# Kernel optimization log

Hardware: AMD Instinct MI355X
Metric: run time of the kernel (lower is better)

## Reference

```python
import jax, jax.numpy as jnp
import numpy as np

N, T, D, H = 2, 2048, 1024, 16
DH = D // H  # per-head dim = 64


def setup_inputs() -> dict:
    key = jax.random.key(0)
    k1, k2, k3, k4 = jax.random.split(key, 4)
    x = jax.random.normal(k1, (N, T, D), dtype=jnp.float32)
    W = jax.random.normal(k2, (D, 3 * D), dtype=jnp.float32) * (D ** -0.5)
    proj_w = jax.random.normal(k3, (D, D), dtype=jnp.float32) * (D ** -0.5)
    proj_b = jax.random.normal(k4, (D,), dtype=jnp.float32) * 0.02
    return {"x": x, "W": W, "proj_w": proj_w, "proj_b": proj_b}


def reference(x, W, proj_w, proj_b):
    n, t, d = x.shape
    qkv = x @ W                                   # [N,T,3D]
    q, k, v = jnp.split(qkv, 3, axis=-1)          # each [N,T,D]
    def heads(a):
        return a.reshape(n, t, H, DH).transpose(0, 2, 1, 3)  # [N,H,T,DH]
    q, k, v = heads(q), heads(k), heads(v)
    scale = DH ** -0.5
    scores = jnp.einsum('nhtd,nhsd->nhts', q, k) * scale      # [N,H,T,T]
    causal = jnp.tril(jnp.ones((t, t), dtype=bool))
    scores = jnp.where(causal, scores, jnp.finfo(scores.dtype).min)
    w = jax.nn.softmax(scores, axis=-1)
    out = jnp.einsum('nhts,nhsd->nhtd', w, v)                 # [N,H,T,DH]
    out = out.transpose(0, 2, 1, 3).reshape(n, t, d)          # [N,T,D]
    return out @ proj_w.T + proj_b
```

## Files before the change

kernel.cpp:

```cpp
#include <hip/hip_runtime.h>
#include <hip/hip_bf16.h>
#include <stdint.h>

#define N_B 2
#define T_S 2048
#define D_M 1024
#define H_N 16
#define D_H 64

typedef __bf16 bf16_t;
typedef __bf16 bf16x8 __attribute__((ext_vector_type(8)));
typedef float f32x4 __attribute__((ext_vector_type(4)));

__device__ __forceinline__ void async_ld16(const void* g, void* lds_uniform_base) {
  __builtin_amdgcn_global_load_lds(
      (const __attribute__((address_space(1))) uint32_t*)(uintptr_t)g,
      (__attribute__((address_space(3))) uint32_t*)(uintptr_t)lds_uniform_base,
      16, 0, 0);
}

__global__ __launch_bounds__(256) void cvt_kernel(const float* __restrict__ in,
                                                  bf16_t* __restrict__ out, int n4) {
  int i = blockIdx.x * blockDim.x + threadIdx.x;
  if (i < n4) {
    float4 v = ((const float4*)in)[i];
    union { bf16_t b[4]; uint64_t u; } o;
    o.b[0] = (bf16_t)v.x; o.b[1] = (bf16_t)v.y;
    o.b[2] = (bf16_t)v.z; o.b[3] = (bf16_t)v.w;
    *(uint64_t*)(out + (size_t)i * 4) = o.u;
  }
}

__global__ __launch_bounds__(256) void transpose_cvt_kernel(const float* __restrict__ in,
                                                            bf16_t* __restrict__ out,
                                                            int R, int C) {
  __shared__ float tile[32][33];
  int bx = blockIdx.x * 32;
  int by = blockIdx.y * 32;
  int tx = threadIdx.x, ty = threadIdx.y;
#pragma unroll
  for (int i = 0; i < 32; i += 8)
    tile[ty + i][tx] = in[(size_t)(by + ty + i) * C + bx + tx];
  __syncthreads();
#pragma unroll
  for (int i = 0; i < 32; i += 8)
    out[(size_t)(bx + ty + i) * R + by + tx] = (bf16_t)tile[tx][ty + i];
}

template <int MODE>
__global__ __launch_bounds__(256) void gemm_bt_kernel(
    const bf16_t* __restrict__ A, const bf16_t* __restrict__ Bt,
    bf16_t* __restrict__ Qo, bf16_t* __restrict__ Ko, bf16_t* __restrict__ Vto,
    const float* __restrict__ bias, float* __restrict__ Co,
    int nbx, int cpx) {
  __shared__ bf16_t As[128 * 32];
  __shared__ bf16_t Bs[128 * 32];
  const int tid = threadIdx.x;
  const int lane = tid & 63;
  const int wid = tid >> 6;
  const int wr = wid >> 1, wc = wid & 1;
  const int g = lane >> 4, lr = lane & 15;
  const int d_ = blockIdx.x;
  const int orig = (d_ & 7) * cpx + (d_ >> 3);
  const int brow = (orig / nbx) * 128;
  const int bcol = (orig % nbx) * 128;

  f32x4 acc[4][4] = {};

  for (int k0 = 0; k0 < 1024; k0 += 32) {
#pragma unroll
    for (int q = 0; q < 2; ++q) {
      int idx = wid * 128 + q * 64 + lane;
      int row = idx >> 2, part = (idx & 3) * 8;
      async_ld16(A + (size_t)(brow + row) * 1024 + k0 + part,
                 &As[(wid * 128 + q * 64) * 8]);
      async_ld16(Bt + (size_t)(bcol + row) * 1024 + k0 + part,
                 &Bs[(wid * 128 + q * 64) * 8]);
    }
    __syncthreads();
    bf16x8 af[4], bfr[4];
#pragma unroll
    for (int i = 0; i < 4; ++i) {
      af[i]  = *(const bf16x8*)&As[(wr * 64 + i * 16 + lr) * 32 + g * 8];
      bfr[i] = *(const bf16x8*)&Bs[(wc * 64 + i * 16 + lr) * 32 + g * 8];
    }
#pragma unroll
    for (int i = 0; i < 4; ++i)
#pragma unroll
      for (int j = 0; j < 4; ++j)
        acc[i][j] = __builtin_amdgcn_mfma_f32_16x16x32_bf16(af[i], bfr[j], acc[i][j], 0, 0, 0);
    __syncthreads();
  }

#pragma unroll
  for (int i = 0; i < 4; ++i) {
    int row0 = brow + wr * 64 + i * 16 + g * 4;
#pragma unroll
    for (int j = 0; j < 4; ++j) {
      int col = bcol + wc * 64 + j * 16 + lr;
#pragma unroll
      for (int r = 0; r < 4; ++r) {
        int row = row0 + r;
        float v = acc[i][j][r];
        if (MODE == 0) {
          int n = row >> 11, t = row & (T_S - 1);
          int which = col >> 10, d = col & (D_M - 1);
          int h = d >> 6, dh = d & 63;
          if (which == 0)
            Qo[((size_t)(n * H_N + h) * T_S + t) * D_H + dh] = (bf16_t)v;
          else if (which == 1)
            Ko[((size_t)(n * H_N + h) * T_S + t) * D_H + dh] = (bf16_t)v;
          else
            Vto[((size_t)(n * H_N + h) * D_H + dh) * T_S + t] = (bf16_t)v;
        } else {
          Co[(size_t)row * D_M + col] = v + bias[col];
        }
      }
    }
  }
}

__global__ __launch_bounds__(256) void attn_kernel(const bf16_t* __restrict__ Q,
                                                   const bf16_t* __restrict__ K,
                                                   const bf16_t* __restrict__ Vt,
                                                   bf16_t* __restrict__ O) {
  __shared__ bf16_t Ks[2][4096];
  __shared__ bf16_t Vs[2][4096];
  __shared__ bf16_t Ps[4][1024];

  const int tid = threadIdx.x;
  const int lane = tid & 63;
  const int w = tid >> 6;
  const int g = lane >> 4, lr = lane & 15;

  const int d_ = blockIdx.x;
  const int x = d_ & 7;
  const int s = d_ >> 3;
  const int hs = s & 3, j_ = s >> 2;
  const int t_ = j_ >> 3, m_ = j_ & 7;
  const int qc = (t_ == 0) ? (31 - m_) : (t_ == 1) ? (16 + m_)
               : (t_ == 2) ? (15 - m_) : m_;
  const int nh = x * 4 + hs;
  const bf16_t* Qg = Q + (size_t)nh * T_S * D_H;
  const char* Kb = (const char*)(K + (size_t)nh * T_S * D_H);
  const char* Vb = (const char*)(Vt + (size_t)nh * D_H * T_S);
  const int n = nh >> 4, h = nh & 15;

  const int c0 = (w * 2 + 0) * 64 + lane;
  const int c1 = (w * 2 + 1) * 64 + lane;
  const int r0 = c0 >> 3, cb0 = (c0 & 7) * 16, sw0 = (r0 & 7) << 4;
  const int r1 = c1 >> 3, cb1 = (c1 & 7) * 16, sw1 = (r1 & 7) << 4;
  const int koff0 = r0 * 128 + (cb0 ^ sw0), koff1 = r1 * 128 + (cb1 ^ sw1);
  const int voff0 = r0 * 4096 + (cb0 ^ sw0), voff1 = r1 * 4096 + (cb1 ^ sw1);
  const int lds0 = (w * 2 + 0) * 1024, lds1 = (w * 2 + 1) * 1024;

  const int q0 = qc * 64 + w * 16;
  const int nt = qc + 1;

  bf16x8 qf[2];
#pragma unroll
  for (int ks = 0; ks < 2; ++ks) {
    bf16x8 t = *(const bf16x8*)(Qg + (size_t)(q0 + lr) * D_H + ks * 32 + g * 8);
#pragma unroll
    for (int e = 0; e < 8; ++e) t[e] = (bf16_t)((float)t[e] * 0.125f);
    qf[ks] = t;
  }

  bf16x8 onesf;
#pragma unroll
  for (int e = 0; e < 8; ++e) onesf[e] = (bf16_t)1.0f;

  f32x4 o_acc[4] = {};
  f32x4 lacc = {};

  auto issue = [&](int t, int b) {
    const char* kt_ = Kb + (size_t)t * 8192;
    const char* vt_ = Vb + (size_t)t * 128;
    async_ld16(kt_ + koff0, (char*)Ks[b] + lds0);
    async_ld16(kt_ + koff1, (char*)Ks[b] + lds1);
    async_ld16(vt_ + voff0, (char*)Vs[b] + lds0);
    async_ld16(vt_ + voff1, (char*)Vs[b] + lds1);
  };

  auto compute = [&](int kt, int b, bool domask) {
    f32x4 s_[4];
    __builtin_amdgcn_s_setprio(1);
#pragma unroll
    for (int j = 0; j < 4; ++j) {
      f32x4 a = {};
#pragma unroll
      for (int ks = 0; ks < 2; ++ks) {
        int row = j * 16 + lr;
        int cb = (ks * 32 + g * 8) * 2;
        bf16x8 kf = *(const bf16x8*)((char*)Ks[b] + ((row * 128 + cb) ^ ((row & 7) << 4)));
        a = __builtin_amdgcn_mfma_f32_16x16x32_bf16(qf[ks], kf, a, 0, 0, 0);
      }
      s_[j] = a;
    }
    __builtin_amdgcn_s_setprio(0);

    if (domask) {
#pragma unroll
      for (int j = 0; j < 4; ++j)
#pragma unroll
        for (int r = 0; r < 4; ++r) {
          int kabs = kt * 64 + j * 16 + lr;
          int qabs = q0 + g * 4 + r;
          if (kabs > qabs) s_[j][r] = -1.0e30f;
        }
    }

#pragma unroll
    for (int j = 0; j < 4; ++j)
#pragma unroll
      for (int r = 0; r < 4; ++r) {
        float sv = fminf(s_[j][r] * 1.442695041f, 50.f);
        float p = __builtin_amdgcn_exp2f(sv);
        int row = g * 4 + r;
        int cb = (j * 16 + lr) * 2;
        *(bf16_t*)((char*)Ps[w] + ((row * 128 + cb) ^ ((row & 7) << 4))) = (bf16_t)p;
      }

    bf16x8 pf[2];
#pragma unroll
    for (int ks = 0; ks < 2; ++ks) {
      int cb = (ks * 32 + g * 8) * 2;
      pf[ks] = *(const bf16x8*)((char*)Ps[w] + ((lr * 128 + cb) ^ ((lr & 7) << 4)));
    }
    __builtin_amdgcn_s_setprio(1);
#pragma unroll
    for (int d = 0; d < 4; ++d) {
#pragma unroll
      for (int ks = 0; ks < 2; ++ks) {
        int row = d * 16 + lr;
        int cb = (ks * 32 + g * 8) * 2;
        bf16x8 vf = *(const bf16x8*)((char*)Vs[b] + ((row * 128 + cb) ^ ((row & 7) << 4)));
        o_acc[d] = __builtin_amdgcn_mfma_f32_16x16x32_bf16(pf[ks], vf, o_acc[d], 0, 0, 0);
      }
    }
#pragma unroll
    for (int ks = 0; ks < 2; ++ks)
      lacc = __builtin_amdgcn_mfma_f32_16x16x32_bf16(pf[ks], onesf, lacc, 0, 0, 0);
    __builtin_amdgcn_s_setprio(0);
  };

  issue(0, 0);
  int buf = 0;
  for (int kt = 0; kt < nt; ++kt) {
    asm volatile("s_waitcnt vmcnt(0)" ::: "memory");
    __builtin_amdgcn_s_barrier();
    __builtin_amdgcn_sched_barrier(0);
    if (kt + 1 < nt) issue(kt + 1, buf ^ 1);
    compute(kt, buf, kt == nt - 1);
    buf ^= 1;
  }

#pragma unroll
  for (int r = 0; r < 4; ++r) {
    int t = q0 + g * 4 + r;
    float inv = 1.f / lacc[r];
#pragma unroll
    for (int d = 0; d < 4; ++d)
      O[(size_t)(n * T_S + t) * D_M + h * D_H + d * 16 + lr] = (bf16_t)(o_acc[d][r] * inv);
  }
}

extern "C" void kernel_launch(void* const* d_in, const int* in_sizes, int n_in,
                              void* d_out, int out_size, void* d_ws, size_t ws_size,
                              hipStream_t stream) {
  const float* x  = (const float*)d_in[0];
  const float* W  = (const float*)d_in[1];
  const float* pw = (const float*)d_in[2];
  const float* pb = (const float*)d_in[3];
  float* out = (float*)d_out;

  char* ws = (char*)d_ws;
  bf16_t* x_bf = (bf16_t*)(ws);
  bf16_t* Wt   = (bf16_t*)(ws + (8ull  << 20));
  bf16_t* pwb  = (bf16_t*)(ws + (14ull << 20));
  bf16_t* Qh   = (bf16_t*)(ws + (16ull << 20));
  bf16_t* Kh   = (bf16_t*)(ws + (24ull << 20));
  bf16_t* Vth  = (bf16_t*)(ws + (32ull << 20));
  bf16_t* Oa   = (bf16_t*)(ws + (40ull << 20));

  cvt_kernel<<<4096, 256, 0, stream>>>(x, x_bf, (4096 * 1024) / 4);
  transpose_cvt_kernel<<<dim3(96, 32), dim3(32, 8), 0, stream>>>(W, Wt, 1024, 3072);
  cvt_kernel<<<1024, 256, 0, stream>>>(pw, pwb, (1024 * 1024) / 4);

  gemm_bt_kernel<0><<<768, 256, 0, stream>>>(x_bf, Wt, Qh, Kh, Vth, nullptr, nullptr, 24, 96);

  attn_kernel<<<1024, 256, 0, stream>>>(Qh, Kh, Vth, Oa);

  gemm_bt_kernel<1><<<256, 256, 0, stream>>>(Oa, pwb, nullptr, nullptr, nullptr, pb, out, 8, 32);
}
```

Measured before the change: 116.1 us.

## Rework attention with 32x32 MFMA, register-resident P and split-K wave pairs

The attention kernel moves from 16x16x32 to 32x32x16 bf16 MFMA tiles. Each pair of waves now shares 32 query rows and splits the 64-key tile in half, with a final LDS reduction to merge the partial outputs and row sums. The softmax probabilities are repacked in registers with cross-half shuffles instead of a round trip through a per-wave LDS buffer. The row sum is accumulated with scalar adds instead of an extra MFMA against a ones vector. This is meant to cut LDS traffic and MFMA issue overhead, at the cost of the epilogue reduction, extra syncs and more register pressure, with an occupancy hint added to launch bounds.

```diff
diff --git a/kernel.cpp b/kernel.cpp
--- a/kernel.cpp
+++ b/kernel.cpp
@@ -11,6 +11,7 @@
 typedef __bf16 bf16_t;
 typedef __bf16 bf16x8 __attribute__((ext_vector_type(8)));
 typedef float f32x4 __attribute__((ext_vector_type(4)));
+typedef float f32x16 __attribute__((ext_vector_type(16)));
 
 __device__ __forceinline__ void async_ld16(const void* g, void* lds_uniform_base) {
   __builtin_amdgcn_global_load_lds(
@@ -120,18 +121,20 @@
   }
 }
 
-__global__ __launch_bounds__(256) void attn_kernel(const bf16_t* __restrict__ Q,
-                                                   const bf16_t* __restrict__ K,
-                                                   const bf16_t* __restrict__ Vt,
-                                                   bf16_t* __restrict__ O) {
+__global__ __launch_bounds__(256, 4) void attn_kernel(const bf16_t* __restrict__ Q,
+                                                      const bf16_t* __restrict__ K,
+                                                      const bf16_t* __restrict__ Vt,
+                                                      bf16_t* __restrict__ O) {
   __shared__ bf16_t Ks[2][4096];
   __shared__ bf16_t Vs[2][4096];
-  __shared__ bf16_t Ps[4][1024];
+  __shared__ float Linv[64];
 
   const int tid = threadIdx.x;
   const int lane = tid & 63;
   const int w = tid >> 6;
-  const int g = lane >> 4, lr = lane & 15;
+  const int qsub = w >> 1, khalf = w & 1;
+  const int l31 = lane & 31;
+  const int hi = lane >> 5;
 
   const int d_ = blockIdx.x;
   const int x = d_ & 7;
@@ -148,30 +151,40 @@
 
   const int c0 = (w * 2 + 0) * 64 + lane;
   const int c1 = (w * 2 + 1) * 64 + lane;
-  const int r0 = c0 >> 3, cb0 = (c0 & 7) * 16, sw0 = (r0 & 7) << 4;
-  const int r1 = c1 >> 3, cb1 = (c1 & 7) * 16, sw1 = (r1 & 7) << 4;
-  const int koff0 = r0 * 128 + (cb0 ^ sw0), koff1 = r1 * 128 + (cb1 ^ sw1);
-  const int voff0 = r0 * 4096 + (cb0 ^ sw0), voff1 = r1 * 4096 + (cb1 ^ sw1);
+  const int r0_ = c0 >> 3, cb0 = (c0 & 7) * 16, sw0 = (r0_ & 7) << 4;
+  const int r1_ = c1 >> 3, cb1 = (c1 & 7) * 16, sw1 = (r1_ & 7) << 4;
+  const int koff0 = r0_ * 128 + (cb0 ^ sw0), koff1 = r1_ * 128 + (cb1 ^ sw1);
+  const int voff0 = r0_ * 4096 + (cb0 ^ sw0), voff1 = r1_ * 4096 + (cb1 ^ sw1);
   const int lds0 = (w * 2 + 0) * 1024, lds1 = (w * 2 + 1) * 1024;
 
-  const int q0 = qc * 64 + w * 16;
+  const int q0w = qc * 64 + qsub * 32;
   const int nt = qc + 1;
 
-  bf16x8 qf[2];
-#pragma unroll
-  for (int ks = 0; ks < 2; ++ks) {
-    bf16x8 t = *(const bf16x8*)(Qg + (size_t)(q0 + lr) * D_H + ks * 32 + g * 8);
+  bf16x8 qf[4];
+#pragma unroll
+  for (int ksd = 0; ksd < 4; ++ksd) {
+    bf16x8 t = *(const bf16x8*)(Qg + (size_t)(q0w + l31) * D_H + ksd * 16 + hi * 8);
 #pragma unroll
     for (int e = 0; e < 8; ++e) t[e] = (bf16_t)((float)t[e] * 0.125f);
-    qf[ks] = t;
-  }
-
-  bf16x8 onesf;
-#pragma unroll
-  for (int e = 0; e < 8; ++e) onesf[e] = (bf16_t)1.0f;
-
-  f32x4 o_acc[4] = {};
-  f32x4 lacc = {};
+    qf[ksd] = t;
+  }
+
+  const int kabs_ = khalf * 32 + l31;
+  int kfo[4];
+#pragma unroll
+  for (int ksd = 0; ksd < 4; ++ksd)
+    kfo[ksd] = (kabs_ * 128 + ksd * 32 + hi * 16) ^ ((kabs_ & 7) << 4);
+  int vfo[2][2];
+#pragma unroll
+  for (int db = 0; db < 2; ++db)
+#pragma unroll
+    for (int kk = 0; kk < 2; ++kk) {
+      int dd = db * 32 + l31;
+      vfo[db][kk] = (dd * 128 + khalf * 64 + kk * 32 + hi * 16) ^ ((dd & 7) << 4);
+    }
+
+  f32x16 oacc[2] = {};
+  float lsum = 0.f;
 
   auto issue = [&](int t, int b) {
     const char* kt_ = Kb + (size_t)t * 8192;
@@ -183,64 +196,62 @@
   };
 
   auto compute = [&](int kt, int b, bool domask) {
-    f32x4 s_[4];
+    f32x16 S = {};
     __builtin_amdgcn_s_setprio(1);
 #pragma unroll
-    for (int j = 0; j < 4; ++j) {
-      f32x4 a = {};
-#pragma unroll
-      for (int ks = 0; ks < 2; ++ks) {
-        int row = j * 16 + lr;
-        int cb = (ks * 32 + g * 8) * 2;
-        bf16x8 kf = *(const bf16x8*)((char*)Ks[b] + ((row * 128 + cb) ^ ((row & 7) << 4)));
-        a = __builtin_amdgcn_mfma_f32_16x16x32_bf16(qf[ks], kf, a, 0, 0, 0);
+    for (int ksd = 0; ksd < 4; ++ksd) {
+      bf16x8 kf = *(const bf16x8*)((char*)Ks[b] + kfo[ksd]);
+      S = __builtin_amdgcn_mfma_f32_32x32x16_bf16(kf, qf[ksd], S, 0, 0, 0);
+    }
+    __builtin_amdgcn_s_setprio(0);
+
+    if (domask) {
+#pragma unroll
+      for (int r = 0; r < 16; ++r) {
+        int ktile = khalf * 32 + (r & 3) + 8 * (r >> 2) + 4 * hi;
+        if (kt * 64 + ktile > q0w + l31) S[r] = -1.0e30f;
       }
-      s_[j] = a;
-    }
-    __builtin_amdgcn_s_setprio(0);
-
-    if (domask) {
-#pragma unroll
-      for (int j = 0; j < 4; ++j)
-#pragma unroll
-        for (int r = 0; r < 4; ++r) {
-          int kabs = kt * 64 + j * 16 + lr;
-          int qabs = q0 + g * 4 + r;
-          if (kabs > qabs) s_[j][r] = -1.0e30f;
-        }
-    }
-
-#pragma unroll
-    for (int j = 0; j < 4; ++j)
-#pragma unroll
-      for (int r = 0; r < 4; ++r) {
-        float sv = fminf(s_[j][r] * 1.442695041f, 50.f);
-        float p = __builtin_amdgcn_exp2f(sv);
-        int row = g * 4 + r;
-        int cb = (j * 16 + lr) * 2;
-        *(bf16_t*)((char*)Ps[w] + ((row * 128 + cb) ^ ((row & 7) << 4))) = (bf16_t)p;
+    }
+
+    float p[16];
+#pragma unroll
+    for (int r = 0; r < 16; ++r) {
+      p[r] = __builtin_amdgcn_exp2f(fminf(S[r] * 1.442695041f, 50.f));
+      lsum += p[r];
+    }
+
+    uint32_t dw[8];
+#pragma unroll
+    for (int i = 0; i < 8; ++i) {
+      union { bf16_t b2[2]; uint32_t u; } pk;
+      pk.b2[0] = (bf16_t)p[2 * i];
+      pk.b2[1] = (bf16_t)p[2 * i + 1];
+      dw[i] = pk.u;
+    }
+
+    bf16x8 pa[2];
+#pragma unroll
+    for (int kk = 0; kk < 2; ++kk) {
+      uint32_t u0 = dw[kk * 4 + 0], u1 = dw[kk * 4 + 1];
+      uint32_t u2 = dw[kk * 4 + 2], u3 = dw[kk * 4 + 3];
+      uint32_t sa = __shfl_xor(hi ? u0 : u2, 32, 64);
+      uint32_t sb = __shfl_xor(hi ? u1 : u3, 32, 64);
+      union { uint32_t u[4]; bf16x8 v; } f;
+      f.u[0] = hi ? sa : u0;
+      f.u[1] = hi ? sb : u1;
+      f.u[2] = hi ? u2 : sa;
+      f.u[3] = hi ? u3 : sb;
+      pa[kk] = f.v;
+    }
+
+    __builtin_amdgcn_s_setprio(1);
+#pragma unroll
+    for (int db = 0; db < 2; ++db)
+#pragma unroll
+      for (int kk = 0; kk < 2; ++kk) {
+        bf16x8 vf = *(const bf16x8*)((char*)Vs[b] + vfo[db][kk]);
+        oacc[db] = __builtin_amdgcn_mfma_f32_32x32x16_bf16(pa[kk], vf, oacc[db], 0, 0, 0);
       }
-
-    bf16x8 pf[2];
-#pragma unroll
-    for (int ks = 0; ks < 2; ++ks) {
-      int cb = (ks * 32 + g * 8) * 2;
-      pf[ks] = *(const bf16x8*)((char*)Ps[w] + ((lr * 128 + cb) ^ ((lr & 7) << 4)));
-    }
-    __builtin_amdgcn_s_setprio(1);
-#pragma unroll
-    for (int d = 0; d < 4; ++d) {
-#pragma unroll
-      for (int ks = 0; ks < 2; ++ks) {
-        int row = d * 16 + lr;
-        int cb = (ks * 32 + g * 8) * 2;
-        bf16x8 vf = *(const bf16x8*)((char*)Vs[b] + ((row * 128 + cb) ^ ((row & 7) << 4)));
-        o_acc[d] = __builtin_amdgcn_mfma_f32_16x16x32_bf16(pf[ks], vf, o_acc[d], 0, 0, 0);
-      }
-    }
-#pragma unroll
-    for (int ks = 0; ks < 2; ++ks)
-      lacc = __builtin_amdgcn_mfma_f32_16x16x32_bf16(pf[ks], onesf, lacc, 0, 0, 0);
     __builtin_amdgcn_s_setprio(0);
   };
 
@@ -255,13 +266,40 @@
     buf ^= 1;
   }
 
-#pragma unroll
-  for (int r = 0; r < 4; ++r) {
-    int t = q0 + g * 4 + r;
-    float inv = 1.f / lacc[r];
-#pragma unroll
-    for (int d = 0; d < 4; ++d)
-      O[(size_t)(n * T_S + t) * D_M + h * D_H + d * 16 + lr] = (bf16_t)(o_acc[d][r] * inv);
+  lsum += __shfl_xor(lsum, 32, 64);
+
+  __syncthreads();
+  float* mO = (float*)Ks;
+  float* mL = (float*)Vs;
+  if (khalf == 1) {
+    float* ob = mO + qsub * 2048;
+#pragma unroll
+    for (int db = 0; db < 2; ++db)
+#pragma unroll
+      for (int r = 0; r < 16; ++r)
+        ob[(db * 16 + r) * 64 + lane] = oacc[db][r];
+    mL[qsub * 32 + l31] = lsum;
+  }
+  __syncthreads();
+  if (khalf == 0) {
+    float* ob = mO + qsub * 2048;
+    float ltot = lsum + mL[qsub * 32 + l31];
+    Linv[qsub * 32 + l31] = 1.f / ltot;
+#pragma unroll
+    for (int db = 0; db < 2; ++db)
+#pragma unroll
+      for (int r = 0; r < 16; ++r)
+        oacc[db][r] += ob[(db * 16 + r) * 64 + lane];
+#pragma unroll
+    for (int r = 0; r < 16; ++r) {
+      int ro = (r & 3) + 8 * (r >> 2) + 4 * hi;
+      int qrow = q0w + ro;
+      float inv = Linv[qsub * 32 + ro];
+#pragma unroll
+      for (int db = 0; db < 2; ++db)
+        O[(size_t)(n * T_S + qrow) * D_M + h * D_H + db * 32 + l31] =
+            (bf16_t)(oacc[db][r] * inv);
+    }
   }
 }
 
```

Result: faster. 109.7 us (-5.6%).
